# Optimization experiments

Hardware: AMD Instinct MI355X
Metric: run time of the kernel (lower is better)

## Reference

```python
import jax, jax.numpy as jnp
import numpy as np

B, S, D, H = 2, 2048, 1024, 16
DH = D // H

def setup_inputs() -> dict:
    key = jax.random.key(0)
    ks = jax.random.split(key, 6)
    scale = 0.02
    return {
        "x":  jax.random.normal(ks[0], (B, S, D), jnp.float32),
        "Wq": jax.random.normal(ks[1], (D, D), jnp.float32) * scale,
        "Wk": jax.random.normal(ks[2], (D, D), jnp.float32) * scale,
        "Wv": jax.random.normal(ks[3], (D, D), jnp.float32) * scale,
        "Wo": jax.random.normal(ks[4], (D, D), jnp.float32) * scale,
        "bo": jnp.zeros((D,), jnp.float32),
    }

def reference(x, Wq, Wk, Wv, Wo, bo):
    b, s, d = x.shape
    h, dh = H, DH
    # projections -> [b, h, s, dh]
    def split_heads(t):
        return t.reshape(b, s, h, dh).transpose(0, 2, 1, 3)
    q = split_heads(x @ Wq)
    k = split_heads(x @ Wk)
    v = split_heads(x @ Wv)
    # scaled causal attention
    scores = jnp.einsum('bhqd,bhkd->bhqk', q, k) / jnp.sqrt(jnp.float32(dh))
    causal = jnp.tril(jnp.ones((s, s), bool))
    scores = jnp.where(causal[None, None], scores, -jnp.inf)
    attn = jax.nn.softmax(scores, axis=-1)
    # dropout p=0.0 -> identity
    ctx = jnp.einsum('bhqk,bhkd->bhqd', attn, v)
    ctx = ctx.transpose(0, 2, 1, 3).reshape(b, s, d)
    return ctx @ Wo + bo
```

## Files before the change

### kernel.cpp

```cpp
#include <hip/hip_runtime.h>


typedef _Float16 f16;
typedef _Float16 f16x8 __attribute__((ext_vector_type(8)));
typedef _Float16 f16x4 __attribute__((ext_vector_type(4)));
typedef float    f32x4 __attribute__((ext_vector_type(4)));

__device__ __forceinline__ void gload16(const void* g, void* l) {
  __builtin_amdgcn_global_load_lds(
      (const __attribute__((address_space(1))) void*)g,
      (__attribute__((address_space(3))) void*)l, 16, 0, 0);
}

__global__ void cvt_x(const float* __restrict__ x, f16* __restrict__ xb) {
  int idx = blockIdx.x * 256 + threadIdx.x;
  float4 v = ((const float4*)x)[idx];
  f16x4 o = { (f16)v.x, (f16)v.y, (f16)v.z, (f16)v.w };
  ((f16x4*)xb)[idx] = o;
}

__global__ void cvt_w(const float* __restrict__ W0, const float* __restrict__ W1,
                      const float* __restrict__ W2, const float* __restrict__ W3,
                      f16* __restrict__ T0, f16* __restrict__ T1,
                      f16* __restrict__ T2, f16* __restrict__ T3) {
  const float* W = blockIdx.z == 0 ? W0 : blockIdx.z == 1 ? W1 : blockIdx.z == 2 ? W2 : W3;
  f16*        Tt = blockIdx.z == 0 ? T0 : blockIdx.z == 1 ? T1 : blockIdx.z == 2 ? T2 : T3;
  __shared__ f16 tile[64][65];
  int tid = threadIdx.x;
  int k0 = blockIdx.y * 64, n0 = blockIdx.x * 64;
  int rr = tid >> 4, cc = (tid & 15) * 4;
#pragma unroll
  for (int p = 0; p < 4; ++p) {
    int r = rr + p * 16;
    float4 v = *(const float4*)(W + (size_t)(k0 + r) * 1024 + n0 + cc);
    tile[r][cc + 0] = (f16)v.x; tile[r][cc + 1] = (f16)v.y;
    tile[r][cc + 2] = (f16)v.z; tile[r][cc + 3] = (f16)v.w;
  }
  __syncthreads();
#pragma unroll
  for (int p = 0; p < 4; ++p) {
    int r = rr + p * 16;
    f16x4 v;
#pragma unroll
    for (int j = 0; j < 4; ++j) v[j] = tile[cc + j][r];
    *(f16x4*)(Tt + (size_t)(n0 + r) * 1024 + k0 + cc) = v;
  }
}

template <int MODE>
__global__ __launch_bounds__(256, 2)
void gemm_k(const f16* __restrict__ A, const f16* __restrict__ Bt,
            f16* __restrict__ oQ, f16* __restrict__ oK, f16* __restrict__ oV,
            float* __restrict__ oO, const float* __restrict__ bias) {
  constexpr int Kd = 1024;
  constexpr int BN = (MODE == 2) ? 64 : 128;
  constexpr int NF = BN / 32;
  __shared__ f16 smem[128 * 64 + BN * 64];
  f16* sA = smem;
  f16* sB = smem + 128 * 64;
  const int tid = threadIdx.x;
  const int lane = tid & 63, wid = tid >> 6;
  const int wr = wid >> 1, wc = wid & 1;
  const int bm = blockIdx.y * 128, bn = blockIdx.x * BN;

  f32x4 acc[4][NF] = {};

  for (int k0 = 0; k0 < Kd; k0 += 64) {
#pragma unroll
    for (int p = 0; p < 4; ++p) {
      int c = p * 256 + tid;
      int row = c >> 3;
      int gc = (c & 7) ^ (row & 7);
      gload16(A + (size_t)(bm + row) * Kd + k0 + gc * 8, sA + c * 8);
    }
#pragma unroll
    for (int p = 0; p < NF; ++p) {
      int c = p * 256 + tid;
      int row = c >> 3;
      int gc = (c & 7) ^ (row & 7);
      gload16(Bt + (size_t)(bn + row) * Kd + k0 + gc * 8, sB + c * 8);
    }
    __syncthreads();
#pragma unroll
    for (int ks = 0; ks < 2; ++ks) {
      f16x8 af[4], bf[NF];
#pragma unroll
      for (int m = 0; m < 4; ++m) {
        int row = wr * 64 + m * 16 + (lane & 15);
        int j = (ks * 4 + (lane >> 4)) ^ (row & 7);
        af[m] = *(const f16x8*)((const char*)sA + row * 128 + j * 16);
      }
#pragma unroll
      for (int n = 0; n < NF; ++n) {
        int row = wc * (BN / 2) + n * 16 + (lane & 15);
        int j = (ks * 4 + (lane >> 4)) ^ (row & 7);
        bf[n] = *(const f16x8*)((const char*)sB + row * 128 + j * 16);
      }
#pragma unroll
      for (int m = 0; m < 4; ++m)
#pragma unroll
        for (int n = 0; n < NF; ++n)
          acc[m][n] = __builtin_amdgcn_mfma_f32_16x16x32_f16(af[m], bf[n], acc[m][n], 0, 0, 0);
    }
    __syncthreads();
  }

  if constexpr (MODE == 2) {
#pragma unroll
    for (int m = 0; m < 4; ++m) {
      int rbase = bm + wr * 64 + m * 16 + ((lane >> 4) << 2);
#pragma unroll
      for (int n = 0; n < NF; ++n) {
        int ncol = bn + wc * (BN / 2) + n * 16 + (lane & 15);
        float bv = bias[ncol];
#pragma unroll
        for (int i = 0; i < 4; ++i)
          oO[(size_t)(rbase + i) * 1024 + ncol] = acc[m][n][i] + bv;
      }
    }
  } else {
    const int seg = bn >> 10;
    if (seg < 2) {
      f16* dst = seg == 0 ? oQ : oK;
#pragma unroll
      for (int m = 0; m < 4; ++m) {
        int rbase = bm + wr * 64 + m * 16 + ((lane >> 4) << 2);
#pragma unroll
        for (int n = 0; n < NF; ++n) {
          int ncol = (bn & 1023) + wc * 64 + n * 16 + (lane & 15);
          int h = ncol >> 6, dh = ncol & 63;
#pragma unroll
          for (int i = 0; i < 4; ++i) {
            int rr = rbase + i;
            int b = rr >> 11, s = rr & 2047;
            dst[(((size_t)(b * 16 + h) * 2048 + s) << 6) + dh] = (f16)acc[m][n][i];
          }
        }
      }
    } else {
      f16* T64 = smem;
      int b = bm >> 11, sbase = bm & 2047;
      int bnl = bn & 1023;
#pragma unroll
      for (int p = 0; p < 2; ++p) {
        if (wr == p) {
#pragma unroll
          for (int m = 0; m < 4; ++m)
#pragma unroll
            for (int n = 0; n < NF; ++n)
#pragma unroll
              for (int i = 0; i < 4; ++i) {
                int rl = m * 16 + ((lane >> 4) << 2) + i;
                int col = wc * 64 + n * 16 + (lane & 15);
                T64[rl * 132 + col] = (f16)acc[m][n][i];
              }
        }
        __syncthreads();
#pragma unroll
        for (int it = 0; it < 4; ++it) {
          int oc = it * 256 + tid;
          int ocol = oc >> 3;
          int och = oc & 7;
          f16x8 v;
#pragma unroll
          for (int j = 0; j < 8; ++j) v[j] = T64[(och * 8 + j) * 132 + ocol];
          int ncol = bnl + ocol;
          int h = ncol >> 6, dh = ncol & 63;
          *(f16x8*)(oV + ((size_t)((b * 16 + h) * 64 + dh) << 11) + sbase + p * 64 + och * 8) = v;
        }
        __syncthreads();
      }
    }
  }
}

__global__ __launch_bounds__(256, 2)
void attn_k(const f16* __restrict__ Q, const f16* __restrict__ Kg,
            const f16* __restrict__ Vt, f16* __restrict__ ctx) {
  __shared__ f16 sK[128 * 64];
  __shared__ f16 sV[64 * 128];
  __shared__ f16 sP[4][16 * 64];
  const int tid = threadIdx.x, lane = tid & 63, wid = tid >> 6;
  const int bh = blockIdx.y;
  const int b = bh >> 4, h = bh & 15;
  const int qt = ((bh >> 3) & 1) ? (31 - (int)blockIdx.x) : (int)blockIdx.x;
  const f16* Qb = Q + ((size_t)bh << 17);
  const f16* Kb = Kg + ((size_t)bh << 17);
  const f16* Vb = Vt + ((size_t)bh << 17);
  const float SC = 0.1803368801f;

  const int qbase = qt * 64 + wid * 16;
  const int qg = qbase + (lane & 15);
  const int qmax_w = qbase + 15;

  f16x8 qf[2];
  {
    const f16* qp = Qb + (size_t)(qbase + (lane & 15)) * 64 + ((lane >> 4) << 3);
    qf[0] = *(const f16x8*)(qp);
    qf[1] = *(const f16x8*)(qp + 32);
  }

  f32x4 acc[4] = {};
  float m_run = -INFINITY, l_run = 0.f;
  const int nkt = (qt >> 1) + 1;

  for (int kt = 0; kt < nkt; ++kt) {
#pragma unroll
    for (int p = 0; p < 4; ++p) {
      int c = p * 256 + tid;
      int row = c >> 3;
      int gc = (c & 7) ^ (row & 7);
      gload16(Kb + (size_t)(kt * 128 + row) * 64 + gc * 8, sK + c * 8);
    }
#pragma unroll
    for (int p = 0; p < 4; ++p) {
      int c = p * 256 + tid;
      int drow = c >> 4;
      int gc = (c & 15) ^ (drow & 7);
      gload16(Vb + (size_t)drow * 2048 + kt * 128 + gc * 8, sV + c * 8);
    }
    __syncthreads();

    char* Pw = (char*)(sP[wid]);
#pragma unroll
    for (int sub = 0; sub < 2; ++sub) {
      const int koff = kt * 128 + sub * 64;
      if (koff > qmax_w) break;

      f32x4 sf[4];
#pragma unroll
      for (int kc = 0; kc < 4; ++kc) {
        if (koff + kc * 16 <= qmax_w) {
          f32x4 z = {};
#pragma unroll
          for (int ks = 0; ks < 2; ++ks) {
            int row = sub * 64 + kc * 16 + (lane & 15);
            int j = (ks * 4 + (lane >> 4)) ^ (row & 7);
            f16x8 kf = *(const f16x8*)((const char*)sK + row * 128 + j * 16);
            z = __builtin_amdgcn_mfma_f32_16x16x32_f16(kf, qf[ks], z, 0, 0, 0);
          }
          sf[kc] = z;
        } else {
          sf[kc] = (f32x4){-1e30f, -1e30f, -1e30f, -1e30f};
        }
      }
#pragma unroll
      for (int kc = 0; kc < 4; ++kc) {
        if (koff + kc * 16 + 15 > qbase) {
#pragma unroll
          for (int i = 0; i < 4; ++i) {
            int kg = koff + kc * 16 + ((lane >> 4) << 2) + i;
            sf[kc][i] = (kg <= qg) ? sf[kc][i] * SC : -1e30f;
          }
        } else {
#pragma unroll
          for (int i = 0; i < 4; ++i) sf[kc][i] *= SC;
        }
      }
      float v01 = fmaxf(fmaxf(sf[0][0], sf[0][1]), fmaxf(sf[0][2], sf[0][3]));
      float v23 = fmaxf(fmaxf(sf[1][0], sf[1][1]), fmaxf(sf[1][2], sf[1][3]));
      float v45 = fmaxf(fmaxf(sf[2][0], sf[2][1]), fmaxf(sf[2][2], sf[2][3]));
      float v67 = fmaxf(fmaxf(sf[3][0], sf[3][1]), fmaxf(sf[3][2], sf[3][3]));
      float v = fmaxf(fmaxf(v01, v23), fmaxf(v45, v67));
      v = fmaxf(v, __shfl_xor(v, 16));
      v = fmaxf(v, __shfl_xor(v, 32));
      float mn = fmaxf(m_run, v);
      float scl = __builtin_amdgcn_exp2f(m_run - mn);
      m_run = mn;
      float ls = 0.f;
#pragma unroll
      for (int kc = 0; kc < 4; ++kc)
#pragma unroll
        for (int i = 0; i < 4; ++i) {
          float p = __builtin_amdgcn_exp2f(sf[kc][i] - mn);
          sf[kc][i] = p;
          ls += p;
        }
      ls += __shfl_xor(ls, 16);
      ls += __shfl_xor(ls, 32);
      l_run = l_run * scl + ls;
#pragma unroll
      for (int i = 0; i < 4; ++i) {
        float sb = __shfl(scl, ((lane >> 4) << 2) + i);
#pragma unroll
        for (int d = 0; d < 4; ++d) acc[d][i] *= sb;
      }
#pragma unroll
      for (int kc = 0; kc < 4; ++kc) {
        int kbase = kc * 16 + ((lane >> 4) << 2);
        int ch = kbase >> 3;
        f16x4 pv = { (f16)sf[kc][0], (f16)sf[kc][1], (f16)sf[kc][2], (f16)sf[kc][3] };
        *(f16x4*)(Pw + (lane & 15) * 128 + ((ch ^ (lane & 7)) << 4) + ((kbase & 7) << 1)) = pv;
      }
#pragma unroll
      for (int kk = 0; kk < 2; ++kk) {
        if (koff + kk * 32 <= qmax_w) {
          int prow = lane & 15;
          int pj = (kk * 4 + (lane >> 4)) ^ (prow & 7);
          f16x8 pa = *(const f16x8*)(Pw + prow * 128 + pj * 16);
#pragma unroll
          for (int d = 0; d < 4; ++d) {
            int vrow = d * 16 + (lane & 15);
            int vch = (sub * 8 + kk * 4 + (lane >> 4)) ^ (vrow & 7);
            f16x8 vf = *(const f16x8*)((const char*)sV + vrow * 256 + vch * 16);
            acc[d] = __builtin_amdgcn_mfma_f32_16x16x32_f16(pa, vf, acc[d], 0, 0, 0);
          }
        }
      }
    }
    __syncthreads();
  }
#pragma unroll
  for (int i = 0; i < 4; ++i) {
    float lb = __shfl(l_run, ((lane >> 4) << 2) + i);
    float r = 1.f / lb;
    int s = qbase + ((lane >> 4) << 2) + i;
#pragma unroll
    for (int d = 0; d < 4; ++d) {
      float val = acc[d][i] * r;
      ctx[((size_t)(b * 2048 + s) << 10) + (h << 6) + (d << 4) + (lane & 15)] = (f16)val;
    }
  }
}

extern "C" void kernel_launch(void* const* d_in, const int* in_sizes, int n_in,
                              void* d_out, int out_size, void* d_ws, size_t ws_size,
                              hipStream_t stream) {
  const float* x  = (const float*)d_in[0];
  const float* Wq = (const float*)d_in[1];
  const float* Wk = (const float*)d_in[2];
  const float* Wv = (const float*)d_in[3];
  const float* Wo = (const float*)d_in[4];
  const float* bo = (const float*)d_in[5];
  char* ws = (char*)d_ws;
  f16* xb   = (f16*)(ws);
  f16* Wcat = (f16*)(ws + ((size_t)8  << 20));
  f16* Wot  = (f16*)(ws + ((size_t)14 << 20));
  f16* Qb   = (f16*)(ws + ((size_t)16 << 20));
  f16* Kb   = (f16*)(ws + ((size_t)24 << 20));
  f16* Vtb  = (f16*)(ws + ((size_t)32 << 20));
  f16* ctx  = (f16*)(ws + ((size_t)40 << 20));
  const size_t MM = (size_t)1024 * 1024;

  hipLaunchKernelGGL(cvt_x, dim3(4096), dim3(256), 0, stream, x, xb);
  hipLaunchKernelGGL(cvt_w, dim3(16, 16, 4), dim3(256), 0, stream,
                     Wq, Wk, Wv, Wo, Wcat, Wcat + MM, Wcat + 2 * MM, Wot);
  hipLaunchKernelGGL((gemm_k<0>), dim3(24, 32), dim3(256), 0, stream,
                     xb, Wcat, Qb, Kb, Vtb, nullptr, nullptr);
  hipLaunchKernelGGL(attn_k, dim3(32, 32), dim3(256), 0, stream, Qb, Kb, Vtb, ctx);
  hipLaunchKernelGGL((gemm_k<2>), dim3(16, 32), dim3(256), 0, stream,
                     ctx, Wot, nullptr, nullptr, nullptr, (float*)d_out, bo);
}
```

Measured before the change: 186.6 us.

## Fold softmax scale into Q, use lazy max rescaling, and compute row sums via MFMA

Pre-multiplies Q by the softmax scale so the per-score multiply is dropped. The running max is only updated when some row's max exceeds it by more than a threshold (lazy rescaling), which skips the accumulator rescale on most tiles. The row-sum reduction with shuffles is replaced by an extra MFMA of P against a ones vector. This adds an MFMA per P chunk and risks fp16 precision from scaling Q and from exponentials up to 2^8 before normalization.

```diff
diff --git a/kernel.cpp b/kernel.cpp
--- a/kernel.cpp
+++ b/kernel.cpp
@@ -196,12 +196,19 @@
   f16x8 qf[2];
   {
     const f16* qp = Qb + (size_t)(qbase + (lane & 15)) * 64 + ((lane >> 4) << 3);
-    qf[0] = *(const f16x8*)(qp);
-    qf[1] = *(const f16x8*)(qp + 32);
-  }
-
+    f16x8 r0 = *(const f16x8*)(qp);
+    f16x8 r1 = *(const f16x8*)(qp + 32);
+#pragma unroll
+    for (int j = 0; j < 8; ++j) {
+      qf[0][j] = (f16)((float)r0[j] * SC);
+      qf[1][j] = (f16)((float)r1[j] * SC);
+    }
+  }
+
+  const f16x8 ones = { (f16)1, (f16)1, (f16)1, (f16)1, (f16)1, (f16)1, (f16)1, (f16)1 };
   f32x4 acc[4] = {};
-  float m_run = -INFINITY, l_run = 0.f;
+  f32x4 lacc = {};
+  float m_run = -INFINITY;
   const int nkt = (qt >> 1) + 1;
 
   for (int kt = 0; kt < nkt; ++kt) {
@@ -250,11 +257,8 @@
 #pragma unroll
           for (int i = 0; i < 4; ++i) {
             int kg = koff + kc * 16 + ((lane >> 4) << 2) + i;
-            sf[kc][i] = (kg <= qg) ? sf[kc][i] * SC : -1e30f;
+            if (kg > qg) sf[kc][i] = -1e30f;
           }
-        } else {
-#pragma unroll
-          for (int i = 0; i < 4; ++i) sf[kc][i] *= SC;
         }
       }
       float v01 = fmaxf(fmaxf(sf[0][0], sf[0][1]), fmaxf(sf[0][2], sf[0][3]));
@@ -264,32 +268,26 @@
       float v = fmaxf(fmaxf(v01, v23), fmaxf(v45, v67));
       v = fmaxf(v, __shfl_xor(v, 16));
       v = fmaxf(v, __shfl_xor(v, 32));
-      float mn = fmaxf(m_run, v);
-      float scl = __builtin_amdgcn_exp2f(m_run - mn);
-      m_run = mn;
-      float ls = 0.f;
-#pragma unroll
-      for (int kc = 0; kc < 4; ++kc)
+      if (!__all(v <= m_run + 8.f)) {
+        float mn = fmaxf(m_run, v);
+        float scl = __builtin_amdgcn_exp2f(m_run - mn);
+        m_run = mn;
 #pragma unroll
         for (int i = 0; i < 4; ++i) {
-          float p = __builtin_amdgcn_exp2f(sf[kc][i] - mn);
-          sf[kc][i] = p;
-          ls += p;
-        }
-      ls += __shfl_xor(ls, 16);
-      ls += __shfl_xor(ls, 32);
-      l_run = l_run * scl + ls;
-#pragma unroll
-      for (int i = 0; i < 4; ++i) {
-        float sb = __shfl(scl, ((lane >> 4) << 2) + i);
-#pragma unroll
-        for (int d = 0; d < 4; ++d) acc[d][i] *= sb;
+          float sb = __shfl(scl, ((lane >> 4) << 2) + i);
+#pragma unroll
+          for (int d = 0; d < 4; ++d) acc[d][i] *= sb;
+          lacc[i] *= sb;
+        }
       }
 #pragma unroll
       for (int kc = 0; kc < 4; ++kc) {
         int kbase = kc * 16 + ((lane >> 4) << 2);
         int ch = kbase >> 3;
-        f16x4 pv = { (f16)sf[kc][0], (f16)sf[kc][1], (f16)sf[kc][2], (f16)sf[kc][3] };
+        f16x4 pv;
+#pragma unroll
+        for (int i = 0; i < 4; ++i)
+          pv[i] = (f16)__builtin_amdgcn_exp2f(sf[kc][i] - m_run);
         *(f16x4*)(Pw + (lane & 15) * 128 + ((ch ^ (lane & 7)) << 4) + ((kbase & 7) << 1)) = pv;
       }
 #pragma unroll
@@ -298,6 +296,7 @@
           int prow = lane & 15;
           int pj = (kk * 4 + (lane >> 4)) ^ (prow & 7);
           f16x8 pa = *(const f16x8*)(Pw + prow * 128 + pj * 16);
+          lacc = __builtin_amdgcn_mfma_f32_16x16x32_f16(pa, ones, lacc, 0, 0, 0);
 #pragma unroll
           for (int d = 0; d < 4; ++d) {
             int vrow = d * 16 + (lane & 15);
@@ -312,8 +311,7 @@
   }
 #pragma unroll
   for (int i = 0; i < 4; ++i) {
-    float lb = __shfl(l_run, ((lane >> 4) << 2) + i);
-    float r = 1.f / lb;
+    float r = 1.f / lacc[i];
     int s = qbase + ((lane >> 4) << 2) + i;
 #pragma unroll
     for (int d = 0; d < 4; ++d) {
```

New measurement: 181.1 us. 3.0% less time.
